# Kernel optimization log

Measured on AMD Instinct MI355X. Metric: run time of the kernel, lower is better.

Reference implementation:

```python
import jax, jax.numpy as jnp
import numpy as np

NUM_HEADS = 8
EPS = 1e-12  # torch F.normalize eps


def setup_inputs() -> dict:
    key = jax.random.key(0)
    k1, k2, k3 = jax.random.split(key, 3)
    B, N, C = 8, 4096, 768
    x = jax.random.normal(k1, (B, N, C), dtype=jnp.float32)
    Wqkv = jax.random.normal(k2, (C, 3 * C), dtype=jnp.float32) * 0.02
    temperature = jnp.ones((NUM_HEADS, 1, 1), dtype=jnp.float32)
    Wproj = jax.random.normal(k3, (C, C), dtype=jnp.float32) * 0.02
    bproj = jnp.zeros((C,), dtype=jnp.float32)
    return {"x": x, "Wqkv": Wqkv, "temperature": temperature,
            "Wproj": Wproj, "bproj": bproj}


def _l2norm(t):
    # torch F.normalize(dim=-1): x / max(||x||, eps)
    n = jnp.sqrt(jnp.sum(t * t, axis=-1, keepdims=True))
    return t / jnp.maximum(n, EPS)


def reference(x, Wqkv, temperature, Wproj, bproj):
    B, N, C = x.shape
    H = NUM_HEADS
    Ch = C // H
    qkv = (x @ Wqkv).reshape(B, N, 3, H, Ch)
    qkv = qkv.transpose(2, 0, 3, 1, 4)           # (3, B, H, N, Ch)
    q, k, v = qkv[0], qkv[1], qkv[2]
    # transpose(-2,-1): attend over channels -> (B, H, Ch, N)
    q = jnp.swapaxes(q, -2, -1)
    k = jnp.swapaxes(k, -2, -1)
    v = jnp.swapaxes(v, -2, -1)
    q = _l2norm(q)
    k = _l2norm(k)
    # (B, H, Ch, Ch) channel-attention scores, scaled by learned temperature
    attn = jnp.einsum('bhcn,bhdn->bhcd', q, k) * temperature
    attn = jax.nn.softmax(attn, axis=-1)
    out = jnp.einsum('bhcd,bhdn->bhcn', attn, v)  # (B, H, Ch, N)
    out = out.transpose(0, 3, 1, 2).reshape(B, N, C)
    return out @ Wproj + bproj
```

## Files before the change

### kernel.cpp

```cpp
#include <hip/hip_runtime.h>
#include <cstdint>
#include <cstddef>

typedef unsigned short u16;
typedef short bf16x8 __attribute__((ext_vector_type(8)));
typedef unsigned short u16x4 __attribute__((ext_vector_type(4)));
typedef unsigned short u16x8 __attribute__((ext_vector_type(8)));
typedef float f32x4 __attribute__((ext_vector_type(4)));

#define EPSN 1e-12f

__device__ __forceinline__ u16 f2bf(float f) {
  uint32_t u = __builtin_bit_cast(uint32_t, f);
  u += 0x7FFFu + ((u >> 16) & 1u);
  return (u16)(u >> 16);
}
__device__ __forceinline__ float bf2f(u16 h) {
  uint32_t u = ((uint32_t)h) << 16;
  return __builtin_bit_cast(float, u);
}

__device__ __forceinline__ void gll16(const u16* g, u16* l) {
  __builtin_amdgcn_global_load_lds(
      (const __attribute__((address_space(1))) void*)g,
      (__attribute__((address_space(3))) void*)l, 16, 0, 0);
}

__global__ __launch_bounds__(256)
void k_cvtT(const float* __restrict__ x, u16* __restrict__ Xh,
            u16* __restrict__ XhT) {
  __shared__ u16 tr[64][68];
  const int tid = threadIdx.x;
  const int t0 = blockIdx.x * 64, k0 = blockIdx.y * 64, b = blockIdx.z;
  const int rq = tid >> 4;
  const int cq = tid & 15;
  const size_t base = ((size_t)b * 4096 + t0) * 768 + k0;
  u16 m[4][4];
#pragma unroll
  for (int e = 0; e < 4; e++) {
    const int r = rq * 4 + e;
    f32x4 v = *(const f32x4*)(x + base + (size_t)r * 768 + cq * 4);
    u16x4 o;
#pragma unroll
    for (int q = 0; q < 4; q++) o[q] = f2bf(v[q]);
    *(u16x4*)(Xh + base + (size_t)r * 768 + cq * 4) = o;
    m[e][0] = o[0]; m[e][1] = o[1]; m[e][2] = o[2]; m[e][3] = o[3];
  }
#pragma unroll
  for (int q = 0; q < 4; q++) {
    u16x4 w;
    w[0] = m[0][q]; w[1] = m[1][q]; w[2] = m[2][q]; w[3] = m[3][q];
    *(u16x4*)&tr[cq * 4 + q][rq * 4] = w;
  }
  __syncthreads();
  const size_t tbase = ((size_t)b * 768 + k0) * 4096 + t0;
#pragma unroll
  for (int p = 0; p < 4; p++) {
    const int kk = (tid >> 4) + p * 16;
    const int ts = (tid & 15) * 4;
    u16x4 o = *(const u16x4*)&tr[kk][ts];
    *(u16x4*)(XhT + tbase + (size_t)kk * 4096 + ts) = o;
  }
}

__global__ __launch_bounds__(256)
void k_wt(const float* __restrict__ W, u16* __restrict__ Wt, u16* __restrict__ Wvh) {
  __shared__ float tile[32][33];
  const int j0 = blockIdx.x * 32;
  const int k0 = blockIdx.y * 32;
  const int tx = threadIdx.x & 31;
  const int ty = threadIdx.x >> 5;
#pragma unroll
  for (int r = 0; r < 4; r++) {
    float v = W[(size_t)(k0 + ty + r * 8) * 2304 + j0 + tx];
    tile[ty + r * 8][tx] = v;
    if (j0 >= 1536)
      Wvh[(size_t)(k0 + ty + r * 8) * 768 + (j0 - 1536) + tx] = f2bf(v);
  }
  __syncthreads();
  if (j0 < 1536) {
#pragma unroll
    for (int r = 0; r < 4; r++)
      Wt[(size_t)(j0 + ty + r * 8) * 768 + k0 + tx] = f2bf(tile[tx][ty + r * 8]);
  }
}

template <int OUTF32B, int TRI>
__global__ __launch_bounds__(256, 3)
void k_gemm(const u16* __restrict__ A, const u16* __restrict__ Btp,
            void* __restrict__ Cp, const float* __restrict__ bias,
            int K, int lda, int ldb, int ldc,
            long aZ, long bZ, long cZ, int zK, long kss) {
  const int gx = gridDim.x, gy = gridDim.y;
  int f = blockIdx.x + gx * (blockIdx.y + gy * blockIdx.z);
  const int total = gx * gy * gridDim.z;
  const int q = total >> 3, rr = total & 7;
  const int xcd = f & 7, kk0 = f >> 3;
  f = (xcd < rr ? xcd * (q + 1) : rr * (q + 1) + (xcd - rr) * q) + kk0;
  const int bx = f % gx;
  const int tmp = f / gx;
  const int by = tmp % gy;
  const int bz = tmp / gy;

  int m0, n0;
  if constexpr (TRI) {
    const int ty = (bx >= 20) ? 5 : (bx >= 18) ? 4 : (bx >= 15) ? 3
                 : (bx >= 11) ? 2 : (bx >= 6) ? 1 : 0;
    const int txi = ty + (bx - (ty * 6 - (ty * (ty - 1)) / 2));
    m0 = ty * 128;
    n0 = txi * 128;
  } else {
    m0 = by * 128;
    n0 = bx * 128;
  }
  const int z = bz;
  const int bb = z / zK, ss = z % zK;
  const u16* Az = A + (long)bb * aZ + (long)ss * kss;
  const u16* Btz = Btp + (long)bb * bZ + (long)ss * kss;

  __shared__ u16 As[3 * 128 * 32];
  __shared__ u16 Bs[3 * 128 * 32];
  const int tid = threadIdx.x;
  const int lane = tid & 63;
  const int wid = tid >> 6;
  const int wr = wid >> 1, wc = wid & 1;
  const int fm = lane & 15, kg = lane >> 4;

  const int lr = lane >> 2;
  const int gk = (lane & 3) ^ ((lane >> 3) & 3);
  const u16* gA = Az + (size_t)(m0 + wid * 32 + lr) * lda + gk * 8;
  const u16* gB = Btz + (size_t)(n0 + wid * 32 + lr) * ldb + gk * 8;
  const size_t a16 = (size_t)16 * lda, b16 = (size_t)16 * ldb;
  u16* lA = As + wid * 1024;
  u16* lB = Bs + wid * 1024;
  const int kq = (kg ^ ((fm >> 1) & 3)) * 8;

  auto STAGE = [&](int slot, int ko) {
    u16* la = lA + slot * 4096;
    u16* lb = lB + slot * 4096;
    gll16(gA + ko, la);
    gll16(gA + ko + a16, la + 512);
    gll16(gB + ko, lb);
    gll16(gB + ko + b16, lb + 512);
  };

  const int nt = K >> 5;
  STAGE(0, 0);
  STAGE(1, 32);
  int sC = 0, sN = 1, sS = 2;

  f32x4 acc[4][4] = {};
  for (int t = 0; t < nt; ++t) {
    if (t + 2 < nt) {
      STAGE(sS, (t + 2) * 32);
      __builtin_amdgcn_sched_barrier(0);
      asm volatile("s_waitcnt vmcnt(8)" ::: "memory");
    } else if (t + 2 == nt) {
      asm volatile("s_waitcnt vmcnt(4)" ::: "memory");
    } else {
      asm volatile("s_waitcnt vmcnt(0)" ::: "memory");
    }
    __builtin_amdgcn_sched_barrier(0);
    __builtin_amdgcn_s_barrier();
    __builtin_amdgcn_sched_barrier(0);

    const u16* as_ = As + sC * 4096;
    const u16* bs_ = Bs + sC * 4096;
    bf16x8 af[4], bfr[4];
#pragma unroll
    for (int i = 0; i < 4; i++)
      af[i] = *(const bf16x8*)&as_[(wr * 64 + i * 16 + fm) * 32 + kq];
#pragma unroll
    for (int j = 0; j < 4; j++)
      bfr[j] = *(const bf16x8*)&bs_[(wc * 64 + j * 16 + fm) * 32 + kq];
    asm volatile("s_waitcnt lgkmcnt(0)" ::: "memory");
    __builtin_amdgcn_sched_barrier(0);
    __builtin_amdgcn_s_barrier();
    __builtin_amdgcn_sched_barrier(0);

#pragma unroll
    for (int i = 0; i < 4; i++)
#pragma unroll
      for (int j = 0; j < 4; j++)
        acc[i][j] = __builtin_amdgcn_mfma_f32_16x16x32_bf16(af[i], bfr[j], acc[i][j], 0, 0, 0);

    const int t2 = sC; sC = sN; sN = sS; sS = t2;
  }

  if constexpr (OUTF32B) {
    float* C = (float*)Cp + (long)z * cZ;
#pragma unroll
    for (int j = 0; j < 4; j++) {
      const int col = n0 + wc * 64 + j * 16 + fm;
      const float bj = bias[col];
#pragma unroll
      for (int i = 0; i < 4; i++) {
        const int r0 = m0 + wr * 64 + i * 16 + kg * 4;
#pragma unroll
        for (int r = 0; r < 4; r++)
          C[(size_t)(r0 + r) * ldc + col] = acc[i][j][r] + bj;
      }
    }
  } else {
    const int rb = TRI ? 0 : m0;
    const int cb = TRI ? 0 : n0;
    const int ld = TRI ? 128 : ldc;
    u16* C = (u16*)Cp + (long)z * cZ + (TRI ? (long)bx * 16384 : 0L);
#pragma unroll
    for (int j = 0; j < 4; j++) {
      const int col = cb + wc * 64 + j * 16 + fm;
#pragma unroll
      for (int i = 0; i < 4; i++) {
        const int r0 = rb + wr * 64 + i * 16 + kg * 4;
#pragma unroll
        for (int r = 0; r < 4; r++)
          C[(size_t)(r0 + r) * ld + col] = f2bf(acc[i][j][r]);
      }
    }
  }
}

template <int OUTF32B>
__global__ __launch_bounds__(512, 4)
void k_gemm2(const u16* __restrict__ A, const u16* __restrict__ Btp,
             void* __restrict__ Cp, const float* __restrict__ bias,
             int K, int lda, int ldb, int ldc,
             long aZ, long bZ, long cZ) {
  const int gx = gridDim.x, gy = gridDim.y;
  int f = blockIdx.x + gx * (blockIdx.y + gy * blockIdx.z);
  const int total = gx * gy * gridDim.z;
  const int q = total >> 3, rr = total & 7;
  const int xcd = f & 7, kk0 = f >> 3;
  f = (xcd < rr ? xcd * (q + 1) : rr * (q + 1) + (xcd - rr) * q) + kk0;
  const int bx = f % gx;
  const int tmp = f / gx;
  const int by = tmp % gy;
  const int bz = tmp / gy;

  const int m0 = by * 256, n0 = bx * 128;
  const u16* Az = A + (long)bz * aZ;
  const u16* Btz = Btp + (long)bz * bZ;

  __shared__ u16 As[2][256 * 32];
  __shared__ u16 Bs[2][128 * 32];
  const int tid = threadIdx.x;
  const int lane = tid & 63;
  const int wid = tid >> 6;
  const int wr = wid & 3, wc = wid >> 2;
  const int fm = lane & 15, kg = lane >> 4;

  const int lr = lane >> 2;
  const int gk = (lane & 3) ^ ((lane >> 3) & 3);
  const u16* gA = Az + (size_t)(m0 + wid * 32 + lr) * lda + gk * 8;
  const u16* gB = Btz + (size_t)(n0 + wid * 16 + lr) * ldb + gk * 8;
  const size_t a16 = (size_t)16 * lda;
  const int kq = (kg ^ ((fm >> 1) & 3)) * 8;

  auto STAGE = [&](int s, int ko) {
    u16* la = &As[s][wid * 1024];
    u16* lb = &Bs[s][wid * 512];
    gll16(gA + ko, la);
    gll16(gA + ko + a16, la + 512);
    gll16(gB + ko, lb);
  };

  const int nt = K >> 5;
  STAGE(0, 0);
  int cur = 0;

  f32x4 acc[4][4] = {};
  for (int t = 0; t < nt; ++t) {
    __syncthreads();
    bf16x8 af[4], bfr[4];
#pragma unroll
    for (int i = 0; i < 4; i++)
      af[i] = *(const bf16x8*)&As[cur][(wr * 64 + i * 16 + fm) * 32 + kq];
#pragma unroll
    for (int j = 0; j < 4; j++)
      bfr[j] = *(const bf16x8*)&Bs[cur][(wc * 64 + j * 16 + fm) * 32 + kq];
    if (t + 1 < nt) STAGE(cur ^ 1, (t + 1) * 32);
#pragma unroll
    for (int i = 0; i < 4; i++)
#pragma unroll
      for (int j = 0; j < 4; j++)
        acc[i][j] = __builtin_amdgcn_mfma_f32_16x16x32_bf16(af[i], bfr[j], acc[i][j], 0, 0, 0);
    cur ^= 1;
  }

  if constexpr (OUTF32B) {
    float* C = (float*)Cp + (long)bz * cZ;
#pragma unroll
    for (int j = 0; j < 4; j++) {
      const int col = n0 + wc * 64 + j * 16 + fm;
      const float bj = bias[col];
#pragma unroll
      for (int i = 0; i < 4; i++) {
        const int r0 = m0 + wr * 64 + i * 16 + kg * 4;
#pragma unroll
        for (int r = 0; r < 4; r++)
          C[(size_t)(r0 + r) * ldc + col] = acc[i][j][r] + bj;
      }
    }
  } else {
    u16* C = (u16*)Cp + (long)bz * cZ;
#pragma unroll
    for (int j = 0; j < 4; j++) {
      const int col = n0 + wc * 64 + j * 16 + fm;
#pragma unroll
      for (int i = 0; i < 4; i++) {
        const int r0 = m0 + wr * 64 + i * 16 + kg * 4;
#pragma unroll
        for (int r = 0; r < 4; r++)
          C[(size_t)(r0 + r) * ldc + col] = f2bf(acc[i][j][r]);
      }
    }
  }
}

__global__ __launch_bounds__(256)
void k_red(const u16* __restrict__ P, u16* __restrict__ O) {
  const int b = blockIdx.y;
  const int ti = blockIdx.x / 6, tj = blockIdx.x % 6;
  const bool mirror = ti > tj;
  const int a = mirror ? tj : ti;
  const int c2 = mirror ? ti : tj;
  const int src = a * 6 - (a * (a - 1)) / 2 + (c2 - a);
  __shared__ u16 lt[128 * 128];
  const int tid = threadIdx.x;
  const int r = tid >> 1;
  const int ch = (tid & 1) * 64;
  float acc[64] = {};
  for (int s = 0; s < 4; s++) {
    const u16* p = P + ((size_t)(b * 4 + s) * 344064 + (size_t)src * 16384);
    __syncthreads();
#pragma unroll
    for (int it = 0; it < 8; it++) {
      const int idx = (tid + it * 256) * 8;
      *(u16x8*)&lt[idx] = *(const u16x8*)(p + idx);
    }
    __syncthreads();
    if (!mirror) {
#pragma unroll
      for (int e = 0; e < 64; e++) acc[e] += bf2f(lt[r * 128 + ch + e]);
    } else {
#pragma unroll
      for (int e = 0; e < 64; e++) acc[e] += bf2f(lt[(ch + e) * 128 + r]);
    }
  }
  u16* o = O + (size_t)b * 589824 + (size_t)(ti * 128 + r) * 768 + tj * 128 + ch;
#pragma unroll
  for (int v8 = 0; v8 < 8; v8++) {
    u16x8 w;
#pragma unroll
    for (int e = 0; e < 8; e++) w[e] = f2bf(acc[v8 * 8 + e]);
    *(u16x8*)(o + v8 * 8) = w;
  }
}

__global__ __launch_bounds__(256)
void k_score(const u16* __restrict__ Tm, const u16* __restrict__ Wt,
             const float* __restrict__ temperature, float* __restrict__ Aattn) {
  const int h = blockIdx.x, b = blockIdx.y;
  const int bh = b * 8 + h;
  __shared__ u16 As[96 * 32];
  __shared__ u16 Bs[96 * 32];
  __shared__ u16 Dt2[96 * 32];
  __shared__ u16 Dwq[96 * 32];
  __shared__ float Gs[96 * 96];
  __shared__ float nqs[96], nks[96], invk[96];

  const int tid = threadIdx.x;
  const int lane = tid & 63;
  const int wid = tid >> 6;
  const int wr = wid >> 1, wc = wid & 1;
  const int fm = lane & 15, kg = lane >> 4;
  const int lr = lane >> 2;
  const int gkS = (lane & 3) ^ ((lane >> 3) & 3);
  const int gkL = (lane & 3);
  const int kq = (kg ^ ((fm >> 1) & 3)) * 8;

  const u16* baseT1 = Tm + (size_t)b * 1179648 + (size_t)(h * 96) * 768;
  const u16* baseT2 = baseT1 + (size_t)768 * 768;
  const u16* baseWq = Wt + (size_t)(h * 96) * 768;
  const u16* baseWk = baseWq + (size_t)768 * 768;

  const u16* gsrc;
  u16* ldst;
  int gblk = gkS;
  if (wid == 0) { gsrc = baseT1; ldst = As; }
  else if (wid == 1) { gsrc = baseWk; ldst = Bs; }
  else if (wid == 2) { gsrc = baseT2; ldst = Dt2; gblk = gkL; }
  else { gsrc = baseWq; ldst = Dwq; gblk = gkL; }

  f32x4 acc[3][3] = {};
  float nqa = 0.f, nka = 0.f;
  const int sw1 = (tid < 96) ? ((tid >> 1) & 3) : 0;
  const int sw2 = (tid >= 128 && tid < 224) ? (((tid - 128) >> 1) & 3) : 0;

  for (int k0 = 0; k0 < 768; k0 += 32) {
    __syncthreads();
#pragma unroll
    for (int c = 0; c < 6; c++) {
      gll16(gsrc + (size_t)(c * 16 + lr) * 768 + k0 + gblk * 8,
            ldst + c * 512);
    }
    __syncthreads();
    bf16x8 af[3], bfr[3];
#pragma unroll
    for (int i = 0; i < 3; i++)
      af[i] = *(const bf16x8*)&As[(wr * 48 + i * 16 + fm) * 32 + kq];
#pragma unroll
    for (int j = 0; j < 3; j++)
      bfr[j] = *(const bf16x8*)&Bs[(wc * 48 + j * 16 + fm) * 32 + kq];
#pragma unroll
    for (int i = 0; i < 3; i++)
#pragma unroll
      for (int j = 0; j < 3; j++)
        acc[i][j] = __builtin_amdgcn_mfma_f32_16x16x32_bf16(af[i], bfr[j], acc[i][j], 0, 0, 0);
    if (tid < 96) {
#pragma unroll
      for (int g = 0; g < 4; g++) {
        u16x8 av = *(const u16x8*)&As[tid * 32 + (g ^ sw1) * 8];
        u16x8 w = *(const u16x8*)&Dwq[tid * 32 + g * 8];
#pragma unroll
        for (int e = 0; e < 8; e++) nqa += bf2f(av[e]) * bf2f(w[e]);
      }
    } else if (tid >= 128 && tid < 224) {
      const int d = tid - 128;
#pragma unroll
      for (int g = 0; g < 4; g++) {
        u16x8 av = *(const u16x8*)&Bs[d * 32 + (g ^ sw2) * 8];
        u16x8 w = *(const u16x8*)&Dt2[d * 32 + g * 8];
#pragma unroll
        for (int e = 0; e < 8; e++) nka += bf2f(av[e]) * bf2f(w[e]);
      }
    }
  }

  if (tid < 96) nqs[tid] = nqa;
  if (tid >= 128 && tid < 224) nks[tid - 128] = nka;
#pragma unroll
  for (int i = 0; i < 3; i++)
#pragma unroll
    for (int j = 0; j < 3; j++)
#pragma unroll
      for (int r = 0; r < 4; r++)
        Gs[(wr * 48 + i * 16 + kg * 4 + r) * 96 + wc * 48 + j * 16 + fm] = acc[i][j][r];
  __syncthreads();
  if (tid < 96) invk[tid] = 1.0f / fmaxf(sqrtf(nks[tid]), EPSN);
  __syncthreads();
  if (tid < 96) {
    const int c = tid;
    const float iq = temperature[h] / fmaxf(sqrtf(nqs[c]), EPSN);
    float sv[96];
    float m = -1e30f;
#pragma unroll
    for (int d = 0; d < 96; d++) {
      float s = Gs[c * 96 + d] * iq * invk[d];
      sv[d] = s;
      m = fmaxf(m, s);
    }
    float sum = 0.f;
#pragma unroll
    for (int d = 0; d < 96; d++) {
      float e = __expf(sv[d] - m);
      sv[d] = e;
      sum += e;
    }
    const float inv = 1.0f / sum;
    float* dst = Aattn + (size_t)bh * 9216 + (size_t)c * 96;
#pragma unroll
    for (int d = 0; d < 96; d++) dst[d] = sv[d] * inv;
  }
}

__global__ __launch_bounds__(256)
void k_weff(const float* __restrict__ Aattn, const float* __restrict__ Wproj,
            u16* __restrict__ Weff) {
  const int jt = blockIdx.x, h = blockIdx.y, b = blockIdx.z;
  const int bh = b * 8 + h;
  __shared__ float As2[9216];
  const int tid = threadIdx.x;
  for (int idx = tid; idx < 9216; idx += 256)
    As2[idx] = Aattn[(size_t)bh * 9216 + idx];
  __syncthreads();
  const int jloc = tid & 127;
  const int half = tid >> 7;
  const int j = jt * 128 + jloc;
  float acc[48] = {};
  for (int c = 0; c < 96; c++) {
    const float w = Wproj[(size_t)(h * 96 + c) * 768 + j];
    const f32x4* ar = (const f32x4*)&As2[c * 96 + half * 48];
#pragma unroll
    for (int v4 = 0; v4 < 12; v4++) {
      f32x4 av = ar[v4];
      acc[v4 * 4 + 0] += w * av[0];
      acc[v4 * 4 + 1] += w * av[1];
      acc[v4 * 4 + 2] += w * av[2];
      acc[v4 * 4 + 3] += w * av[3];
    }
  }
  u16* dst = Weff + ((size_t)b * 768 + j) * 768 + h * 96 + half * 48;
#pragma unroll
  for (int v4 = 0; v4 < 12; v4++) {
    u16x4 o;
    o[0] = f2bf(acc[v4 * 4 + 0]);
    o[1] = f2bf(acc[v4 * 4 + 1]);
    o[2] = f2bf(acc[v4 * 4 + 2]);
    o[3] = f2bf(acc[v4 * 4 + 3]);
    *(u16x4*)(dst + v4 * 4) = o;
  }
}

extern "C" void kernel_launch(void* const* d_in, const int* in_sizes, int n_in,
                              void* d_out, int out_size, void* d_ws, size_t ws_size,
                              hipStream_t stream) {
  const float* x = (const float*)d_in[0];
  const float* Wqkv = (const float*)d_in[1];
  const float* temp = (const float*)d_in[2];
  const float* Wproj = (const float*)d_in[3];
  const float* bproj = (const float*)d_in[4];
  float* out = (float*)d_out;

  char* ws = (char*)d_ws;
  u16* Xh = (u16*)ws;
  u16* XhT = (u16*)(ws + 50331648);
  u16* Wt = (u16*)(ws + 100663296);
  u16* Wvh = (u16*)(ws + 103022592);
  u16* XtXp = (u16*)(ws + 104202240);
  u16* XtXbf = (u16*)(ws + 141950976);
  u16* T = (u16*)(ws + 151388160);
  u16* WeffT = (u16*)(ws + 151388160);
  u16* WcompT = (u16*)(ws + 160825344);
  float* Aattn = (float*)(ws + 170262528);

  k_cvtT<<<dim3(64, 12, 8), 256, 0, stream>>>(x, Xh, XhT);
  k_wt<<<dim3(72, 24), 256, 0, stream>>>(Wqkv, Wt, Wvh);
  k_gemm<0, 1><<<dim3(21, 1, 32), 256, 0, stream>>>(
      XhT, XhT, (void*)XtXp, nullptr, 1024, 4096, 4096, 0,
      3145728L, 3145728L, 344064L, 4, 1024L);
  k_red<<<dim3(36, 8), 256, 0, stream>>>(XtXp, XtXbf);
  k_gemm<0, 0><<<dim3(6, 12, 8), 256, 0, stream>>>(
      Wt, XtXbf, (void*)T, nullptr, 768, 768, 768, 768,
      0L, 589824L, 1179648L, 1, 0L);
  k_score<<<dim3(8, 8), 256, 0, stream>>>(T, Wt, temp, Aattn);
  k_weff<<<dim3(6, 8, 8), 256, 0, stream>>>(Aattn, Wproj, WeffT);
  k_gemm<0, 0><<<dim3(6, 6, 8), 256, 0, stream>>>(
      WeffT, Wvh, (void*)WcompT, nullptr, 768, 768, 768, 768,
      589824L, 0L, 589824L, 1, 0L);
  k_gemm2<1><<<dim3(6, 16, 8), 512, 0, stream>>>(
      Xh, WcompT, out, bproj, 768, 768, 768, 768,
      3145728L, 589824L, 3145728L);
}
```

Before: 301.0 us.

## Enlarge final GEMM tile to 256x256 with three-stage LDS pipeline

Replaces the final projection GEMM kernel with a 256x256-tile variant in which each wave computes 128x64, and LDS staging moves from double to triple buffering. Loads are issued two k-steps ahead, with explicit vmcnt waits and barriers in place of the single syncthreads. The goal is more reuse per loaded tile and more hiding of global-load latency. In exchange it uses more LDS and registers (launch bounds drop to 2 blocks per CU) and launches half as many blocks (384), which may hurt occupancy and load balance across CUs.

```diff
diff --git a/kernel.cpp b/kernel.cpp
--- a/kernel.cpp
+++ b/kernel.cpp
@@ -220,10 +220,9 @@
   }
 }
 
-template <int OUTF32B>
-__global__ __launch_bounds__(512, 4)
-void k_gemm2(const u16* __restrict__ A, const u16* __restrict__ Btp,
-             void* __restrict__ Cp, const float* __restrict__ bias,
+__global__ __launch_bounds__(512, 2)
+void k_gemm8(const u16* __restrict__ A, const u16* __restrict__ Btp,
+             float* __restrict__ C, const float* __restrict__ bias,
              int K, int lda, int ldb, int ldc,
              long aZ, long bZ, long cZ) {
   const int gx = gridDim.x, gy = gridDim.y;
@@ -237,82 +236,90 @@
   const int by = tmp % gy;
   const int bz = tmp / gy;
 
-  const int m0 = by * 256, n0 = bx * 128;
+  const int m0 = by * 256, n0 = bx * 256;
   const u16* Az = A + (long)bz * aZ;
   const u16* Btz = Btp + (long)bz * bZ;
 
-  __shared__ u16 As[2][256 * 32];
-  __shared__ u16 Bs[2][128 * 32];
+  __shared__ u16 As[3 * 256 * 32];
+  __shared__ u16 Bs[3 * 256 * 32];
   const int tid = threadIdx.x;
   const int lane = tid & 63;
   const int wid = tid >> 6;
-  const int wr = wid & 3, wc = wid >> 2;
+  const int wm = wid >> 2, wn = wid & 3;
   const int fm = lane & 15, kg = lane >> 4;
 
   const int lr = lane >> 2;
   const int gk = (lane & 3) ^ ((lane >> 3) & 3);
   const u16* gA = Az + (size_t)(m0 + wid * 32 + lr) * lda + gk * 8;
-  const u16* gB = Btz + (size_t)(n0 + wid * 16 + lr) * ldb + gk * 8;
-  const size_t a16 = (size_t)16 * lda;
+  const u16* gB = Btz + (size_t)(n0 + wid * 32 + lr) * ldb + gk * 8;
+  const size_t a16 = (size_t)16 * lda, b16 = (size_t)16 * ldb;
+  u16* lA = As + wid * 1024;
+  u16* lB = Bs + wid * 1024;
   const int kq = (kg ^ ((fm >> 1) & 3)) * 8;
 
-  auto STAGE = [&](int s, int ko) {
-    u16* la = &As[s][wid * 1024];
-    u16* lb = &Bs[s][wid * 512];
+  auto STAGE = [&](int slot, int ko) {
+    u16* la = lA + slot * 8192;
+    u16* lb = lB + slot * 8192;
     gll16(gA + ko, la);
     gll16(gA + ko + a16, la + 512);
     gll16(gB + ko, lb);
+    gll16(gB + ko + b16, lb + 512);
   };
 
   const int nt = K >> 5;
   STAGE(0, 0);
-  int cur = 0;
-
-  f32x4 acc[4][4] = {};
+  STAGE(1, 32);
+  int sC = 0, sN = 1, sS = 2;
+
+  f32x4 acc[8][4] = {};
   for (int t = 0; t < nt; ++t) {
-    __syncthreads();
-    bf16x8 af[4], bfr[4];
-#pragma unroll
-    for (int i = 0; i < 4; i++)
-      af[i] = *(const bf16x8*)&As[cur][(wr * 64 + i * 16 + fm) * 32 + kq];
+    if (t + 2 < nt) {
+      STAGE(sS, (t + 2) * 32);
+      __builtin_amdgcn_sched_barrier(0);
+      asm volatile("s_waitcnt vmcnt(8)" ::: "memory");
+    } else if (t + 2 == nt) {
+      asm volatile("s_waitcnt vmcnt(4)" ::: "memory");
+    } else {
+      asm volatile("s_waitcnt vmcnt(0)" ::: "memory");
+    }
+    __builtin_amdgcn_sched_barrier(0);
+    __builtin_amdgcn_s_barrier();
+    __builtin_amdgcn_sched_barrier(0);
+
+    const u16* as_ = As + sC * 8192;
+    const u16* bs_ = Bs + sC * 8192;
+    bf16x8 af[8], bfr[4];
+#pragma unroll
+    for (int i = 0; i < 8; i++)
+      af[i] = *(const bf16x8*)&as_[(wm * 128 + i * 16 + fm) * 32 + kq];
 #pragma unroll
     for (int j = 0; j < 4; j++)
-      bfr[j] = *(const bf16x8*)&Bs[cur][(wc * 64 + j * 16 + fm) * 32 + kq];
-    if (t + 1 < nt) STAGE(cur ^ 1, (t + 1) * 32);
-#pragma unroll
-    for (int i = 0; i < 4; i++)
+      bfr[j] = *(const bf16x8*)&bs_[(wn * 64 + j * 16 + fm) * 32 + kq];
+    asm volatile("s_waitcnt lgkmcnt(0)" ::: "memory");
+    __builtin_amdgcn_sched_barrier(0);
+    __builtin_amdgcn_s_barrier();
+    __builtin_amdgcn_sched_barrier(0);
+
+#pragma unroll
+    for (int i = 0; i < 8; i++)
 #pragma unroll
       for (int j = 0; j < 4; j++)
         acc[i][j] = __builtin_amdgcn_mfma_f32_16x16x32_bf16(af[i], bfr[j], acc[i][j], 0, 0, 0);
-    cur ^= 1;
-  }
-
-  if constexpr (OUTF32B) {
-    float* C = (float*)Cp + (long)bz * cZ;
-#pragma unroll
-    for (int j = 0; j < 4; j++) {
-      const int col = n0 + wc * 64 + j * 16 + fm;
-      const float bj = bias[col];
-#pragma unroll
-      for (int i = 0; i < 4; i++) {
-        const int r0 = m0 + wr * 64 + i * 16 + kg * 4;
-#pragma unroll
-        for (int r = 0; r < 4; r++)
-          C[(size_t)(r0 + r) * ldc + col] = acc[i][j][r] + bj;
-      }
-    }
-  } else {
-    u16* C = (u16*)Cp + (long)bz * cZ;
-#pragma unroll
-    for (int j = 0; j < 4; j++) {
-      const int col = n0 + wc * 64 + j * 16 + fm;
-#pragma unroll
-      for (int i = 0; i < 4; i++) {
-        const int r0 = m0 + wr * 64 + i * 16 + kg * 4;
-#pragma unroll
-        for (int r = 0; r < 4; r++)
-          C[(size_t)(r0 + r) * ldc + col] = f2bf(acc[i][j][r]);
-      }
+
+    const int t2 = sC; sC = sN; sN = sS; sS = t2;
+  }
+
+  float* Cz = C + (long)bz * cZ;
+#pragma unroll
+  for (int j = 0; j < 4; j++) {
+    const int col = n0 + wn * 64 + j * 16 + fm;
+    const float bj = bias[col];
+#pragma unroll
+    for (int i = 0; i < 8; i++) {
+      const int r0 = m0 + wm * 128 + i * 16 + kg * 4;
+#pragma unroll
+      for (int r = 0; r < 4; r++)
+        Cz[(size_t)(r0 + r) * ldc + col] = acc[i][j][r] + bj;
     }
   }
 }
@@ -548,7 +555,7 @@
   k_gemm<0, 0><<<dim3(6, 6, 8), 256, 0, stream>>>(
       WeffT, Wvh, (void*)WcompT, nullptr, 768, 768, 768, 768,
       589824L, 0L, 589824L, 1, 0L);
-  k_gemm2<1><<<dim3(6, 16, 8), 512, 0, stream>>>(
+  k_gemm8<<<dim3(3, 16, 8), 512, 0, stream>>>(
       Xh, WcompT, out, bproj, 768, 768, 768, 768,
       3145728L, 589824L, 3145728L);
 }
```

New measurement: 321.9 us. 7.0% more time.
